# Kernel tuning notes

Measured on AMD Instinct MI355X. Metric: run time of the kernel, lower is better.

Reference implementation:

```python
import jax, jax.numpy as jnp
import numpy as np

H = 4096          # hidden_size
NIN = 17          # RFSIZE*RFSIZE + ADDINPUT + NBACTIONS = 9+4+4
NA = 4            # NBACTIONS


def setup_inputs() -> dict:
    key = jax.random.key(0)
    ks = jax.random.split(key, 12)
    return {
        "x": jax.random.normal(ks[0], (1, NIN), jnp.float32),
        "hidden": 0.1 * jax.random.normal(ks[1], (1, H), jnp.float32),
        "hebb": 0.01 * jax.random.normal(ks[2], (H, H), jnp.float32),
        "i2h_w": 0.1 * jax.random.normal(ks[3], (H, NIN), jnp.float32),
        "i2h_b": 0.1 * jax.random.normal(ks[4], (H,), jnp.float32),
        "w": 0.01 * jax.random.uniform(ks[5], (H, H), jnp.float32),
        "alpha": 0.01 * jax.random.uniform(ks[6], (H, H), jnp.float32),
        "eta": 0.01 * jnp.ones((1,), jnp.float32),
        "h2o_w": 0.1 * jax.random.normal(ks[7], (NA, H), jnp.float32),
        "h2o_b": 0.1 * jax.random.normal(ks[8], (NA,), jnp.float32),
        "h2v_w": 0.1 * jax.random.normal(ks[9], (1, H), jnp.float32),
        "h2v_b": 0.1 * jax.random.normal(ks[10], (1,), jnp.float32),
    }


def reference(x, hidden, hebb, i2h_w, i2h_b, w, alpha, eta, h2o_w, h2o_b, h2v_w, h2v_b):
    # plastic RNN step: h = tanh(i2h(x) + hidden @ (w + alpha*hebb))
    h = jnp.tanh(x @ i2h_w.T + i2h_b + hidden @ (w + alpha * hebb))  # [1,H]
    # Hebbian trace update: (1-eta)*hebb + eta * outer(hidden, h)
    hebb_new = (1.0 - eta) * hebb + eta * (hidden[0][:, None] * h[0][None, :])  # [H,H]
    activout = jax.nn.softmax(h @ h2o_w.T + h2o_b, axis=-1)  # [1,NA]
    valueout = h @ h2v_w.T + h2v_b                           # [1,1]
    return activout, valueout, h, hebb_new
```

## Files before the change

kernel.cpp:

```cpp
#include <hip/hip_runtime.h>

#define HDIM 4096
#define NIN 17
#define NA 4

using f4 = __attribute__((ext_vector_type(4))) float;

constexpr int TB = 256;
constexpr int CPT = 4;
constexpr int BXC = HDIM / (TB * CPT);
constexpr int NCHUNK = 1024;
constexpr int RPC = HDIM / NCHUNK;
constexpr size_t NELEM = (size_t)HDIM * HDIM;

__global__ void k_matvec(const float* __restrict__ w, const float* __restrict__ alpha,
                         const float* __restrict__ hebb, const float* __restrict__ hidden,
                         float* __restrict__ partial, float* __restrict__ acc5,
                         unsigned* __restrict__ cnt) {
    if (blockIdx.x == 0 && blockIdx.y == 0 && threadIdx.x < 9) {
        if (threadIdx.x < 8) acc5[threadIdx.x] = 0.f;
        else *cnt = 0u;
    }
    const int col0 = (blockIdx.x * TB + threadIdx.x) * CPT;
    const int row0 = blockIdx.y * RPC;
    const size_t base = (size_t)row0 * HDIM + col0;

    f4 wv[RPC], av[RPC], bv[RPC];
#pragma unroll
    for (int r = 0; r < RPC; ++r) {
        const size_t off = base + (size_t)r * HDIM;
        wv[r] = *(const f4*)(w + off);
        av[r] = __builtin_nontemporal_load((const f4*)(alpha + off));
        bv[r] = *(const f4*)(hebb + off);
    }
    f4 acc = {0.f, 0.f, 0.f, 0.f};
#pragma unroll
    for (int r = 0; r < RPC; ++r) {
        const float hv = hidden[row0 + r];
        acc += hv * (wv[r] + av[r] * bv[r]);
    }
    *(f4*)(partial + (size_t)blockIdx.y * HDIM + col0) = acc;
}

constexpr int HC = 32;
constexpr int HGRP = TB / HC;
constexpr int HCPG = NCHUNK / HGRP;

__global__ void k_hact(const float* __restrict__ partial, const float* __restrict__ x,
                       const float* __restrict__ i2h_w, const float* __restrict__ i2h_b,
                       const float* __restrict__ h2o_w, const float* __restrict__ h2o_b,
                       const float* __restrict__ h2v_w, const float* __restrict__ h2v_b,
                       float* __restrict__ h_f, float* __restrict__ h_out,
                       float* __restrict__ acc5, unsigned* __restrict__ cnt,
                       float* __restrict__ out) {
    const int tid = threadIdx.x;
    const int lane = tid & (HC - 1);
    const int grp = tid >> 5;
    const int col = blockIdx.x * HC + lane;

    float s = 0.f;
    const float* p = partial + (size_t)(grp * HCPG) * HDIM + col;
#pragma unroll 16
    for (int c = 0; c < HCPG; ++c) s += p[(size_t)c * HDIM];

    __shared__ float red[TB];
    red[tid] = s;
    __syncthreads();
    for (int st = TB / 2; st >= HC; st >>= 1) {
        if (tid < st) red[tid] += red[tid + st];
        __syncthreads();
    }
    if (tid < HC) {
        float z = red[tid] + i2h_b[col];
#pragma unroll
        for (int k = 0; k < NIN; ++k) z += x[k] * i2h_w[col * NIN + k];
        const float h = tanhf(z);
        h_f[col] = h;
        h_out[col] = h;
        float d[NA + 1];
#pragma unroll
        for (int a = 0; a < NA; ++a) d[a] = h * h2o_w[(size_t)a * HDIM + col];
        d[NA] = h * h2v_w[col];
#pragma unroll
        for (int a = 0; a <= NA; ++a) {
            float v = d[a];
#pragma unroll
            for (int sft = 16; sft > 0; sft >>= 1) v += __shfl_down(v, sft, 32);
            if (lane == 0) atomicAdd(acc5 + a, v);
        }
    }
    if (tid == 0) {
        __threadfence();
        if (atomicAdd(cnt, 1u) == (HDIM / HC) - 1) {
            float res[NA + 1];
#pragma unroll
            for (int a = 0; a <= NA; ++a) res[a] = atomicAdd(acc5 + a, 0.f);
            float o[NA];
            float mx = -1e30f;
#pragma unroll
            for (int a = 0; a < NA; ++a) { o[a] = res[a] + h2o_b[a]; mx = fmaxf(mx, o[a]); }
            float se = 0.f;
#pragma unroll
            for (int a = 0; a < NA; ++a) { o[a] = __expf(o[a] - mx); se += o[a]; }
#pragma unroll
            for (int a = 0; a < NA; ++a) out[a] = o[a] / se;
            out[NA] = res[NA] + h2v_b[0];
        }
    }
}

constexpr size_t NQK = (NELEM - 4) / 4;
constexpr int HEB_BLK = 4096;

__global__ void k_hebb(const float* __restrict__ hebb, const float* __restrict__ hidden,
                       const float* __restrict__ h_f, const float* __restrict__ eta,
                       float* __restrict__ hebb_out) {
    const int tid = threadIdx.x;
    const size_t gt = (size_t)blockIdx.x * TB + tid;
    const size_t wid = gt >> 6;
    const int lane = tid & 63;
    const float e = eta[0];
    const float om = 1.f - e;

    if (gt == 0) {
        const float hv0 = e * hidden[0];
        hebb_out[0] = om * hebb[0] + hv0 * h_f[0];
        hebb_out[1] = om * hebb[1] + hv0 * h_f[1];
        hebb_out[2] = om * hebb[2] + hv0 * h_f[2];
        hebb_out[NELEM - 1] = om * hebb[NELEM - 1] + e * hidden[HDIM - 1] * h_f[HDIM - 1];
    }

    size_t k[4];
    bool ok[4];
    f4 A[4];
#pragma unroll
    for (int q = 0; q < 4; ++q) {
        k[q] = wid * 256 + (size_t)lane + (size_t)q * 64;
        ok[q] = k[q] < NQK;
        A[q] = *(const f4*)(hebb + 4 * k[q]);
    }
    __builtin_amdgcn_sched_barrier(0);

    f4 B[4];
#pragma unroll
    for (int q = 0; q < 4; ++q) {
        B[q].x = __shfl_down(A[q].x, 1, 64);
        B[q].y = __shfl_down(A[q].y, 1, 64);
        B[q].z = __shfl_down(A[q].z, 1, 64);
        B[q].w = 0.f;
    }
    if (lane == 63) {
#pragma unroll
        for (int q = 0; q < 4; ++q)
            if (ok[q]) B[q] = *(const f4*)(hebb + 4 * (k[q] + 1));
    }

#pragma unroll
    for (int q = 0; q < 4; ++q) {
        if (ok[q]) {
            const size_t s = 4 * k[q] + 3;
            const float b[4] = {A[q].w, B[q].x, B[q].y, B[q].z};
            f4 v;
#pragma unroll
            for (int kk = 0; kk < 4; ++kk) {
                const size_t m = s + (size_t)kk;
                const int i = (int)(m >> 12);
                const int jj = (int)(m & (HDIM - 1));
                v[kk] = om * b[kk] + e * hidden[i] * h_f[jj];
            }
            __builtin_nontemporal_store(v, (f4*)(hebb_out + s));
        }
    }
}

extern "C" void kernel_launch(void* const* d_in, const int* in_sizes, int n_in,
                              void* d_out, int out_size, void* d_ws, size_t ws_size,
                              hipStream_t stream) {
    const float* x      = (const float*)d_in[0];
    const float* hidden = (const float*)d_in[1];
    const float* hebb   = (const float*)d_in[2];
    const float* i2h_w  = (const float*)d_in[3];
    const float* i2h_b  = (const float*)d_in[4];
    const float* w      = (const float*)d_in[5];
    const float* alpha  = (const float*)d_in[6];
    const float* eta    = (const float*)d_in[7];
    const float* h2o_w  = (const float*)d_in[8];
    const float* h2o_b  = (const float*)d_in[9];
    const float* h2v_w  = (const float*)d_in[10];
    const float* h2v_b  = (const float*)d_in[11];
    float* out = (float*)d_out;

    float* h_out    = out + 5;
    float* hebb_out = out + 5 + HDIM;

    float* partial = out + 8192;

    float* h_f  = (float*)d_ws;
    float* acc5 = h_f + HDIM;
    unsigned* cnt = (unsigned*)(acc5 + 8);

    k_matvec<<<dim3(BXC, NCHUNK), TB, 0, stream>>>(w, alpha, hebb, hidden, partial, acc5, cnt);
    k_hact<<<HDIM / HC, TB, 0, stream>>>(partial, x, i2h_w, i2h_b, h2o_w, h2o_b,
                                         h2v_w, h2v_b, h_f, h_out, acc5, cnt, out);
    k_hebb<<<HEB_BLK, TB, 0, stream>>>(hebb, hidden, h_f, eta, hebb_out);
}
```

Baseline: 267.5 us.

## Fuse matvec, activation and Hebbian update into one cooperative kernel

Replaces the three-kernel pipeline with a single cooperative-launch kernel using grid-wide syncs. Each thread keeps its hebb tile in registers from the matvec phase and reuses it for the Hebbian update, avoiding a second full read of hebb and two extra launches. The w loads are also made nontemporal. It adds grid sync overhead, higher register pressure, and relies on all blocks being co-resident, with a fallback to the old path otherwise.

```diff
diff --git a/kernel.cpp b/kernel.cpp
--- a/kernel.cpp
+++ b/kernel.cpp
@@ -1,4 +1,7 @@
 #include <hip/hip_runtime.h>
+#include <hip/hip_cooperative_groups.h>
+
+namespace cg = cooperative_groups;
 
 #define HDIM 4096
 #define NIN 17
@@ -7,11 +10,133 @@
 using f4 = __attribute__((ext_vector_type(4))) float;
 
 constexpr int TB = 256;
-constexpr int CPT = 4;
-constexpr int BXC = HDIM / (TB * CPT);
-constexpr int NCHUNK = 1024;
-constexpr int RPC = HDIM / NCHUNK;
 constexpr size_t NELEM = (size_t)HDIM * HDIM;
+
+constexpr int BXC = 4;
+constexpr int NCH = 256;
+constexpr int RPC = HDIM / NCH;
+
+__global__ __launch_bounds__(TB, 4)
+void k_all(const float* __restrict__ w, const float* __restrict__ alpha,
+           const float* __restrict__ hebb, const float* __restrict__ hidden,
+           const float* __restrict__ x, const float* __restrict__ i2h_w,
+           const float* __restrict__ i2h_b,
+           const float* __restrict__ h2o_w, const float* __restrict__ h2o_b,
+           const float* __restrict__ h2v_w, const float* __restrict__ h2v_b,
+           const float* __restrict__ eta,
+           float* __restrict__ partial, float* __restrict__ out,
+           float* __restrict__ acc5) {
+    const int tid = threadIdx.x;
+    const int bx = blockIdx.x;
+    const int by = blockIdx.y;
+    const int col0 = (bx * TB + tid) * 4;
+    const int row0 = by * RPC;
+
+    if (bx == 0 && by == 0 && tid < 8) acc5[tid] = 0.f;
+
+    f4 bv[RPC];
+    f4 acc = {0.f, 0.f, 0.f, 0.f};
+#pragma unroll
+    for (int p = 0; p < RPC / 4; ++p) {
+        f4 wv[4], av[4];
+#pragma unroll
+        for (int rr = 0; rr < 4; ++rr) {
+            const int r = p * 4 + rr;
+            const size_t off = (size_t)(row0 + r) * HDIM + col0;
+            wv[rr] = __builtin_nontemporal_load((const f4*)(w + off));
+            av[rr] = __builtin_nontemporal_load((const f4*)(alpha + off));
+            bv[p * 4 + rr] = *(const f4*)(hebb + off);
+        }
+#pragma unroll
+        for (int rr = 0; rr < 4; ++rr) {
+            const int r = p * 4 + rr;
+            acc += hidden[row0 + r] * (wv[rr] + av[rr] * bv[p * 4 + rr]);
+        }
+    }
+#pragma unroll
+    for (int r = 0; r < RPC; ++r)
+        asm volatile("" : "+v"(bv[r].x), "+v"(bv[r].y), "+v"(bv[r].z), "+v"(bv[r].w));
+
+    *(f4*)(partial + (size_t)by * HDIM + col0) = acc;
+
+    cg::this_grid().sync();
+
+    __shared__ f4 red[TB];
+    const int flat = by * BXC + bx;
+    const int j0 = flat * 4;
+    red[tid] = *(const f4*)(partial + (size_t)tid * HDIM + j0);
+    __syncthreads();
+    for (int s = TB / 2; s > 0; s >>= 1) {
+        if (tid < s) red[tid] += red[tid + s];
+        __syncthreads();
+    }
+    if (tid < 4) {
+        const int j = j0 + tid;
+        float z = red[0][tid] + i2h_b[j];
+#pragma unroll
+        for (int k = 0; k < NIN; ++k) z += x[k] * i2h_w[j * NIN + k];
+        const float h = tanhf(z);
+        out[5 + j] = h;
+        float d[NA + 1];
+#pragma unroll
+        for (int a = 0; a < NA; ++a) d[a] = h * h2o_w[(size_t)a * HDIM + j];
+        d[NA] = h * h2v_w[j];
+#pragma unroll
+        for (int a = 0; a <= NA; ++a) {
+            float v = d[a];
+            v += __shfl_down(v, 2, 4);
+            v += __shfl_down(v, 1, 4);
+            if (tid == 0) atomicAdd(acc5 + a, v);
+        }
+    }
+
+    cg::this_grid().sync();
+
+    if (bx == 0 && by == 0 && tid == 0) {
+        float res[NA + 1];
+#pragma unroll
+        for (int a = 0; a <= NA; ++a) res[a] = atomicAdd(acc5 + a, 0.f);
+        float o[NA];
+        float mx = -1e30f;
+#pragma unroll
+        for (int a = 0; a < NA; ++a) { o[a] = res[a] + h2o_b[a]; mx = fmaxf(mx, o[a]); }
+        float se = 0.f;
+#pragma unroll
+        for (int a = 0; a < NA; ++a) { o[a] = __expf(o[a] - mx); se += o[a]; }
+#pragma unroll
+        for (int a = 0; a < NA; ++a) out[a] = o[a] / se;
+        out[NA] = res[NA] + h2v_b[0];
+    }
+
+    const f4 hv4 = *(const f4*)(out + 5 + col0);
+    const float e = eta[0];
+    const float om = 1.f - e;
+
+    __shared__ f4 sh[2][TB + 1];
+    float* __restrict__ hebb_out = out + 5 + HDIM;
+#pragma unroll 2
+    for (int r = 0; r < RPC; ++r) {
+        const int row = row0 + r;
+        const f4 val = om * bv[r] + (e * hidden[row]) * hv4;
+        f4* sb = sh[r & 1];
+        sb[tid] = val;
+        __syncthreads();
+        float* base = hebb_out + (size_t)row * HDIM + bx * 1024;
+        if (tid < TB - 1) {
+            const f4 v = {sb[tid].w, sb[tid + 1].x, sb[tid + 1].y, sb[tid + 1].z};
+            __builtin_nontemporal_store(v, (f4*)(base + 4 * tid + 3));
+        } else {
+            __builtin_nontemporal_store(sb[0].x, base + 0);
+            __builtin_nontemporal_store(sb[0].y, base + 1);
+            __builtin_nontemporal_store(sb[0].z, base + 2);
+            __builtin_nontemporal_store(sb[TB - 1].w, base + 1023);
+        }
+    }
+}
+
+constexpr int FBXC = 4;
+constexpr int FNCHUNK = 1024;
+constexpr int FRPC = 4;
 
 __global__ void k_matvec(const float* __restrict__ w, const float* __restrict__ alpha,
                          const float* __restrict__ hebb, const float* __restrict__ hidden,
@@ -21,30 +146,26 @@
         if (threadIdx.x < 8) acc5[threadIdx.x] = 0.f;
         else *cnt = 0u;
     }
-    const int col0 = (blockIdx.x * TB + threadIdx.x) * CPT;
-    const int row0 = blockIdx.y * RPC;
+    const int col0 = (blockIdx.x * TB + threadIdx.x) * 4;
+    const int row0 = blockIdx.y * FRPC;
     const size_t base = (size_t)row0 * HDIM + col0;
-
-    f4 wv[RPC], av[RPC], bv[RPC];
-#pragma unroll
-    for (int r = 0; r < RPC; ++r) {
+    f4 wv[FRPC], av[FRPC], bv[FRPC];
+#pragma unroll
+    for (int r = 0; r < FRPC; ++r) {
         const size_t off = base + (size_t)r * HDIM;
-        wv[r] = *(const f4*)(w + off);
+        wv[r] = __builtin_nontemporal_load((const f4*)(w + off));
         av[r] = __builtin_nontemporal_load((const f4*)(alpha + off));
         bv[r] = *(const f4*)(hebb + off);
     }
     f4 acc = {0.f, 0.f, 0.f, 0.f};
 #pragma unroll
-    for (int r = 0; r < RPC; ++r) {
-        const float hv = hidden[row0 + r];
-        acc += hv * (wv[r] + av[r] * bv[r]);
-    }
+    for (int r = 0; r < FRPC; ++r) acc += hidden[row0 + r] * (wv[r] + av[r] * bv[r]);
     *(f4*)(partial + (size_t)blockIdx.y * HDIM + col0) = acc;
 }
 
 constexpr int HC = 32;
 constexpr int HGRP = TB / HC;
-constexpr int HCPG = NCHUNK / HGRP;
+constexpr int HCPG = FNCHUNK / HGRP;
 
 __global__ void k_hact(const float* __restrict__ partial, const float* __restrict__ x,
                        const float* __restrict__ i2h_w, const float* __restrict__ i2h_b,
@@ -57,12 +178,10 @@
     const int lane = tid & (HC - 1);
     const int grp = tid >> 5;
     const int col = blockIdx.x * HC + lane;
-
     float s = 0.f;
     const float* p = partial + (size_t)(grp * HCPG) * HDIM + col;
 #pragma unroll 16
     for (int c = 0; c < HCPG; ++c) s += p[(size_t)c * HDIM];
-
     __shared__ float red[TB];
     red[tid] = s;
     __syncthreads();
@@ -121,7 +240,6 @@
     const int lane = tid & 63;
     const float e = eta[0];
     const float om = 1.f - e;
-
     if (gt == 0) {
         const float hv0 = e * hidden[0];
         hebb_out[0] = om * hebb[0] + hv0 * h_f[0];
@@ -129,10 +247,7 @@
         hebb_out[2] = om * hebb[2] + hv0 * h_f[2];
         hebb_out[NELEM - 1] = om * hebb[NELEM - 1] + e * hidden[HDIM - 1] * h_f[HDIM - 1];
     }
-
-    size_t k[4];
-    bool ok[4];
-    f4 A[4];
+    size_t k[4]; bool ok[4]; f4 A[4];
 #pragma unroll
     for (int q = 0; q < 4; ++q) {
         k[q] = wid * 256 + (size_t)lane + (size_t)q * 64;
@@ -140,7 +255,6 @@
         A[q] = *(const f4*)(hebb + 4 * k[q]);
     }
     __builtin_amdgcn_sched_barrier(0);
-
     f4 B[4];
 #pragma unroll
     for (int q = 0; q < 4; ++q) {
@@ -154,7 +268,6 @@
         for (int q = 0; q < 4; ++q)
             if (ok[q]) B[q] = *(const f4*)(hebb + 4 * (k[q] + 1));
     }
-
 #pragma unroll
     for (int q = 0; q < 4; ++q) {
         if (ok[q]) {
@@ -193,14 +306,29 @@
     float* h_out    = out + 5;
     float* hebb_out = out + 5 + HDIM;
 
-    float* partial = out + 8192;
-
-    float* h_f  = (float*)d_ws;
-    float* acc5 = h_f + HDIM;
+    float* partial = (float*)d_ws;
+    float* acc5 = partial + (size_t)NCH * HDIM;
     unsigned* cnt = (unsigned*)(acc5 + 8);
 
-    k_matvec<<<dim3(BXC, NCHUNK), TB, 0, stream>>>(w, alpha, hebb, hidden, partial, acc5, cnt);
-    k_hact<<<HDIM / HC, TB, 0, stream>>>(partial, x, i2h_w, i2h_b, h2o_w, h2o_b,
-                                         h2v_w, h2v_b, h_f, h_out, acc5, cnt, out);
-    k_hebb<<<HEB_BLK, TB, 0, stream>>>(hebb, hidden, h_f, eta, hebb_out);
-}
+    static int coop = -1;
+    if (coop < 0) {
+        int maxb = 0;
+        hipError_t err = hipOccupancyMaxActiveBlocksPerMultiprocessor(&maxb, k_all, TB, 0);
+        coop = (err == hipSuccess && maxb >= 4) ? 1 : 0;
+    }
+
+    if (coop) {
+        void* args[] = {(void*)&w, (void*)&alpha, (void*)&hebb, (void*)&hidden,
+                        (void*)&x, (void*)&i2h_w, (void*)&i2h_b,
+                        (void*)&h2o_w, (void*)&h2o_b, (void*)&h2v_w, (void*)&h2v_b,
+                        (void*)&eta, (void*)&partial, (void*)&out, (void*)&acc5};
+        hipLaunchCooperativeKernel(k_all, dim3(BXC, NCH), dim3(TB), args, 0, stream);
+    } else {
+        float* fpartial = out + 8192;
+        float* h_f = acc5 + 16;
+        k_matvec<<<dim3(FBXC, FNCHUNK), TB, 0, stream>>>(w, alpha, hebb, hidden, fpartial, acc5, cnt);
+        k_hact<<<HDIM / HC, TB, 0, stream>>>(fpartial, x, i2h_w, i2h_b, h2o_w, h2o_b,
+                                             h2v_w, h2v_b, h_f, h_out, acc5, cnt, out);
+        k_hebb<<<HEB_BLK, TB, 0, stream>>>(hebb, hidden, h_f, eta, hebb_out);
+    }
+}
```

Measured after the change: 260.7 us. 1.03x faster.
